# Kernel optimization log

Measured on AMD Instinct MI355X. Metric: run time of the kernel, lower is better.

## Reference

```python
import jax, jax.numpy as jnp
import numpy as np

D = 128          # embedding dim
N_INIT = 100000  # number of initial (axiom) clauses
L = 64           # topological levels of derived clauses
M = 4096         # derived clauses per level
N_THAX = 2000    # distinct axiom-name (thax) embeddings
N_SINE = 32      # sine-level embeddings
N_RULES = 256    # distinct inference rules (each with its own 2-ary MLP)
N_TOT = N_INIT + L * M


def setup_inputs() -> dict:
    key = jax.random.key(0)
    ks = jax.random.split(key, 10)
    rng = np.random.default_rng(0)
    # parents of level-l nodes point to any node created strictly earlier
    parents = np.stack(
        [rng.integers(0, N_INIT + l * M, size=(M, 2)) for l in range(L)]
    ).astype(np.int32)  # [L, M, 2]
    return {
        "thax_table": jax.random.normal(ks[0], (N_THAX, D), jnp.float32) * 0.1,
        "sine_table": jax.random.normal(ks[1], (N_SINE, D), jnp.float32) * 0.1,
        "rule_W": jax.random.normal(ks[2], (N_RULES, 2 * D, D), jnp.float32) * (1.0 / np.sqrt(2 * D)),
        "rule_b": jax.random.normal(ks[3], (N_RULES, D), jnp.float32) * 0.01,
        "eval_w": jax.random.normal(ks[4], (D,), jnp.float32) * (1.0 / np.sqrt(D)),
        "eval_b": jax.random.normal(ks[5], (1,), jnp.float32) * 0.01,
        "pos_vals": jax.random.uniform(ks[6], (N_TOT,), jnp.float32, 0.01, 1.0),
        "neg_vals": jax.random.uniform(ks[7], (N_TOT,), jnp.float32, 0.01, 1.0),
        "init_thax": jax.random.randint(ks[8], (N_INIT,), 0, N_THAX, jnp.int32),
        "init_sine": jax.random.randint(ks[9], (N_INIT,), 0, N_SINE, jnp.int32),
        "parents": jnp.asarray(parents),
        "rules": jnp.asarray(rng.integers(0, N_RULES, size=(L, M)).astype(np.int32)),
    }


def reference(thax_table, sine_table, rule_W, rule_b, eval_w, eval_b,
              pos_vals, neg_vals, init_thax, init_sine, parents, rules):
    n_init = init_thax.shape[0]
    n_lvl, m = rules.shape
    d = thax_table.shape[1]

    # init nodes: embed = init_embeds[thax]() + sine_embedder(sine)
    init_emb = thax_table[init_thax] + sine_table[init_sine]  # [N_INIT, D]
    store0 = jnp.concatenate(
        [init_emb, jnp.zeros((n_lvl * m, d), init_emb.dtype)], axis=0)  # [N_TOT, D]

    # deriv nodes, level by level: gather 2 parents, per-rule MLP (cat -> Linear -> ReLU)
    def step(store, xs):
        lvl, par, rul = xs                       # par: [M,2] int, rul: [M] int
        pe = store[par].reshape(m, 2 * d)        # gather parent embeddings
        emb = jax.nn.relu(jnp.einsum('mi,mio->mo', pe, rule_W[rul]) + rule_b[rul])
        store = jax.lax.dynamic_update_slice(store, emb, (n_init + lvl * m, 0))
        return store, None

    store, _ = jax.lax.scan(step, store0, (jnp.arange(n_lvl), parents, rules))

    # eval_net + weighted BCEWithLogits (pos_weight = tot_neg / tot_pos)
    logits = store @ eval_w + eval_b[0]          # [N_TOT]
    tot = pos_vals + neg_vals
    y = pos_vals / tot
    pw = jnp.sum(neg_vals) / jnp.sum(pos_vals)
    per_node = pw * y * jax.nn.softplus(-logits) + (1.0 - y) * jax.nn.softplus(logits)
    loss = jnp.sum(tot * per_node).reshape(1)
    posOK = jnp.sum(jnp.where(logits >= 0.0, pos_vals, 0.0))
    negOK = jnp.sum(jnp.where(logits < 0.0, neg_vals, 0.0))
    return (loss, posOK, negOK)
```

## Files before the change

kernel.cpp:

```cpp
#include <hip/hip_runtime.h>

#define D      128
#define NINIT  100000
#define LVLS   64
#define M      4096
#define NRULES 256
#define NTOT   (NINIT + LVLS * M)
#define NTHR   512
#define TILE   32

typedef __attribute__((ext_vector_type(8))) short short8;
typedef __attribute__((ext_vector_type(4))) float floatx4;

#define ST_OFF 256
#define SI_OFF (ST_OFF + (size_t)NTOT * D * 2)
#define RO_OFF (SI_OFF + (size_t)LVLS * M * 4)
#define FL_OFF (RO_OFF + (size_t)LVLS * (NRULES + 1) * 4)

#define CBAR() asm volatile("" ::: "memory")

__device__ __forceinline__ unsigned short f2bf(float x) {
  unsigned u = __float_as_uint(x);
  u += 0x7fffu + ((u >> 16) & 1u);
  return (unsigned short)(u >> 16);
}

__device__ __forceinline__ float softplusf(float x) {
  return fmaxf(x, 0.f) + log1pf(expf(-fabsf(x)));
}

__device__ __forceinline__ void st_sys(unsigned* p, unsigned v) {
  __hip_atomic_store(p, v, __ATOMIC_RELAXED, __HIP_MEMORY_SCOPE_SYSTEM);
}
__device__ __forceinline__ void st_sys64(unsigned long long* p,
                                         unsigned long long v) {
  __hip_atomic_store(p, v, __ATOMIC_RELAXED, __HIP_MEMORY_SCOPE_SYSTEM);
}
__device__ __forceinline__ unsigned ld_sys(const unsigned* p) {
  return __hip_atomic_load(p, __ATOMIC_RELAXED, __HIP_MEMORY_SCOPE_SYSTEM);
}

__device__ __forceinline__ void wait2(const unsigned* f0, bool n0,
                                      const unsigned* f1, bool n1) {
  if (__all(!(n0 || n1))) return;
  unsigned a0 = ld_sys(f0), a1 = ld_sys(f1);
  int guard = 1 << 16;
  for (;;) {
    unsigned b0 = ld_sys(f0), b1 = ld_sys(f1);
    bool ok = (!n0 || a0 != 0u) && (!n1 || a1 != 0u);
    if (__all(ok) || !--guard) break;
    a0 = ld_sys(f0); a1 = ld_sys(f1);
    ok = (!n0 || b0 != 0u) && (!n1 || b1 != 0u);
    if (__all(ok) || !--guard) break;
  }
  CBAR();
}

__device__ __forceinline__ void gbar_light(unsigned* bcnt, unsigned* bgen) {
  __syncthreads();
  if (threadIdx.x == 0) {
    unsigned g = ld_sys(bgen);
    unsigned v = __hip_atomic_fetch_add(bcnt, 1u, __ATOMIC_RELAXED,
                                        __HIP_MEMORY_SCOPE_SYSTEM);
    if (v == gridDim.x - 1) {
      st_sys(bcnt, 0u);
      st_sys(bgen, g + 1u);
    } else {
      int guard = 1 << 22;
      while (ld_sys(bgen) == g && --guard) __builtin_amdgcn_s_sleep(2);
    }
  }
  __syncthreads();
}

__device__ __forceinline__ bool adv_cursor(int r, const int* __restrict__ ro,
                                           int& l, int& t0, int& off, int& cnt) {
  t0 += TILE;
  while (t0 >= cnt) {
    if (++l >= LVLS) return false;
    off = ro[l * (NRULES + 1) + r];
    cnt = ro[l * (NRULES + 1) + r + 1] - off;
    t0 = 0;
  }
  return true;
}

__global__ __launch_bounds__(NTHR, 2) void fused_kernel(
    const float* __restrict__ thax_table, const float* __restrict__ sine_table,
    const float* __restrict__ rule_W, const float* __restrict__ rule_b,
    const float* __restrict__ eval_w, const float* __restrict__ eval_b,
    const float* __restrict__ pos, const float* __restrict__ neg,
    const int* __restrict__ init_thax, const int* __restrict__ init_sine,
    const int* __restrict__ parents,
    const int* __restrict__ rules,
    unsigned short* __restrict__ store, int* __restrict__ sorted_idx,
    int* __restrict__ rule_off, unsigned* __restrict__ flags,
    float* __restrict__ sums, unsigned* __restrict__ bvars,
    float* __restrict__ out) {
  __shared__ unsigned short pe[TILE * 264];
  __shared__ unsigned short ot[TILE * 136];
  __shared__ int s_sid[2][TILE];
  __shared__ int s_cnt[NRULES];
  __shared__ int s_base[NRULES + 1];
  __shared__ float racc[4];

  unsigned* bcnt = bvars;
  unsigned* bgen = bvars + 1;

  const int r = blockIdx.x;
  const int tid = threadIdx.x;
  const int wave = tid >> 6, lane = tid & 63;
  const int col = (wave << 4) + (lane & 15);
  const int node = tid >> 4;
  const int segq = tid & 15;

  float aP1 = 0.f, aP2 = 0.f, a_pos = 0.f, a_neg = 0.f;
  const float eb = eval_b[0];
  float w8[8];
  {
    float4 wA = ((const float4*)eval_w)[segq * 2];
    float4 wB = ((const float4*)eval_w)[segq * 2 + 1];
    w8[0] = wA.x; w8[1] = wA.y; w8[2] = wA.z; w8[3] = wA.w;
    w8[4] = wB.x; w8[5] = wB.y; w8[6] = wB.z; w8[7] = wB.w;
  }

  short8 bf[8];
  {
    const float* Wr = rule_W + (size_t)r * (2 * D * D);
    const int krow_base = (lane >> 4) * 8;
#pragma unroll
    for (int ks = 0; ks < 8; ++ks) {
      union { short8 s; unsigned short us[8]; } c;
#pragma unroll
      for (int j = 0; j < 8; ++j)
        c.us[j] = f2bf(Wr[(size_t)(ks * 32 + krow_base + j) * D + col]);
      bf[ks] = c.s;
    }
  }
  const float bias = rule_b[r * D + col];

  if (r < LVLS) {
    const int l = r;
    const int* rl = rules + (size_t)l * M;
    if (tid < NRULES) s_cnt[tid] = 0;
    __syncthreads();
    for (int m = tid; m < M; m += NTHR) atomicAdd(&s_cnt[rl[m]], 1);
    __syncthreads();
    int c = (tid < NRULES) ? s_cnt[tid] : 0;
    if (tid < NRULES) s_base[tid] = c;
    __syncthreads();
    for (int off = 1; off < NRULES; off <<= 1) {
      int t = (tid < NRULES && tid >= off) ? s_base[tid - off] : 0;
      __syncthreads();
      if (tid < NRULES) s_base[tid] += t;
      __syncthreads();
    }
    if (tid < NRULES) {
      int ex = s_base[tid] - c;
      st_sys((unsigned*)&rule_off[(size_t)l * (NRULES + 1) + tid],
             (unsigned)ex);
      s_cnt[tid] = ex;
    }
    if (tid == 0)
      st_sys((unsigned*)&rule_off[(size_t)l * (NRULES + 1) + NRULES],
             (unsigned)M);
    __syncthreads();
    for (int m = tid; m < M; m += NTHR) {
      int p = atomicAdd(&s_cnt[rl[m]], 1);
      st_sys((unsigned*)&sorted_idx[(size_t)l * M + p], (unsigned)m);
    }
  } else {
    const int gid3 = (r - LVLS) * NTHR + tid;
    const int gstride3 = (NRULES - LVLS) * NTHR;
    for (int idx = gid3; idx < NINIT * 16; idx += gstride3) {
      int nd = idx >> 4, sg = idx & 15;
      const float4* t = (const float4*)(thax_table + (size_t)init_thax[nd] * D) + sg * 2;
      const float4* s = (const float4*)(sine_table + (size_t)init_sine[nd] * D) + sg * 2;
      float4 a0 = t[0], a1 = t[1], b0 = s[0], b1 = s[1];
      float v[8] = {a0.x + b0.x, a0.y + b0.y, a0.z + b0.z, a0.w + b0.w,
                    a1.x + b1.x, a1.y + b1.y, a1.z + b1.z, a1.w + b1.w};
      unsigned p0 = (unsigned)f2bf(v[0]) | ((unsigned)f2bf(v[1]) << 16);
      unsigned p1 = (unsigned)f2bf(v[2]) | ((unsigned)f2bf(v[3]) << 16);
      unsigned p2 = (unsigned)f2bf(v[4]) | ((unsigned)f2bf(v[5]) << 16);
      unsigned p3 = (unsigned)f2bf(v[6]) | ((unsigned)f2bf(v[7]) << 16);
      unsigned long long* dst =
          (unsigned long long*)(store + (size_t)nd * D + sg * 8);
      st_sys64(dst + 0, (unsigned long long)p0 | ((unsigned long long)p1 << 32));
      st_sys64(dst + 1, (unsigned long long)p2 | ((unsigned long long)p3 << 32));

      float pd = v[0] * w8[0] + v[1] * w8[1] + v[2] * w8[2] + v[3] * w8[3] +
                 v[4] * w8[4] + v[5] * w8[5] + v[6] * w8[6] + v[7] * w8[7];
      pd += __shfl_xor(pd, 1, 64);
      pd += __shfl_xor(pd, 2, 64);
      pd += __shfl_xor(pd, 4, 64);
      pd += __shfl_xor(pd, 8, 64);
      if (sg == 0) {
        float logit = pd + eb;
        float pp = pos[nd], nn = neg[nd];
        float tot = pp + nn, y = pp / tot;
        aP1 += tot * y * softplusf(-logit);
        aP2 += tot * (1.f - y) * softplusf(logit);
        if (logit >= 0.f) a_pos += pp; else a_neg += nn;
      }
    }
    float sp = 0.f, sn = 0.f;
    for (int i = gid3; i < NTOT; i += gstride3) {
      sp += pos[i];
      sn += neg[i];
    }
    for (int m = 32; m; m >>= 1) {
      sp += __shfl_xor(sp, m, 64);
      sn += __shfl_xor(sn, m, 64);
    }
    if (lane == 0) {
      atomicAdd(&sums[0], sp);
      atomicAdd(&sums[1], sn);
    }
  }

  gbar_light(bcnt, bgen);

  const float pw = sums[1] / sums[0];

  int lL = -1, t0L = 0, offL = 0, cntL = 0;

  bool validA = adv_cursor(r, rule_off, lL, t0L, offL, cntL);
  int lA = lL, t0A = t0L, cntA = cntL;
  int parA0 = 0, parA1 = 0;
  bool lateA0 = false, lateA1 = false;
  unsigned reA0 = 1u, reA1 = 1u;
  float pPosA = 0.f, pNegA = 0.f;
  uint4 gA0 = {0, 0, 0, 0}, gA1 = {0, 0, 0, 0};
  if (validA) {
    int gj = t0A + node; if (gj > cntA - 1) gj = cntA - 1;
    int sid = sorted_idx[(size_t)lA * M + offL + gj];
    parA0 = parents[((size_t)lA * M + sid) * 2 + 0];
    parA1 = parents[((size_t)lA * M + sid) * 2 + 1];
    pPosA = pos[NINIT + lA * M + sid];
    pNegA = neg[NINIT + lA * M + sid];
    bool n0 = parA0 >= NINIT, n1 = parA1 >= NINIT;
    wait2(flags + (n0 ? parA0 - NINIT : 0), n0,
          flags + (n1 ? parA1 - NINIT : 0), n1);
    gA0 = *(const uint4*)(store + (size_t)parA0 * D + segq * 8);
    gA1 = *(const uint4*)(store + (size_t)parA1 * D + segq * 8);
    if (segq == 0) s_sid[0][node] = sid;
  }

  bool validB = validA && adv_cursor(r, rule_off, lL, t0L, offL, cntL);
  int lB = lL, t0B = t0L, cntB = cntL;
  int sidB = 0, parB0 = 0, parB1 = 0;
  unsigned fB0 = 1u, fB1 = 1u;
  float pPosB = 0.f, pNegB = 0.f;
  if (validB) {
    int gj = t0B + node; if (gj > cntB - 1) gj = cntB - 1;
    sidB = sorted_idx[(size_t)lB * M + offL + gj];
    parB0 = parents[((size_t)lB * M + sidB) * 2 + 0];
    parB1 = parents[((size_t)lB * M + sidB) * 2 + 1];
    fB0 = parB0 >= NINIT ? ld_sys(flags + (parB0 - NINIT)) : 1u;
    fB1 = parB1 >= NINIT ? ld_sys(flags + (parB1 - NINIT)) : 1u;
    pPosB = pos[NINIT + lB * M + sidB];
    pNegB = neg[NINIT + lB * M + sidB];
  }

  bool validC = validB && adv_cursor(r, rule_off, lL, t0L, offL, cntL);
  int lC = lL, t0C = t0L, cntC = cntL;
  int sidC = 0, parC0 = 0, parC1 = 0;
  if (validC) {
    int gj = t0C + node; if (gj > cntC - 1) gj = cntC - 1;
    sidC = sorted_idx[(size_t)lC * M + offL + gj];
    parC0 = parents[((size_t)lC * M + sidC) * 2 + 0];
    parC1 = parents[((size_t)lC * M + sidC) * 2 + 1];
  }

  bool validE = validC && adv_cursor(r, rule_off, lL, t0L, offL, cntL);
  int lE = lL, t0E = t0L, cntE = cntL;
  int sidE = 0;
  if (validE) {
    int gj = t0E + node; if (gj > cntE - 1) gj = cntE - 1;
    sidE = sorted_idx[(size_t)lE * M + offL + gj];
  }

  bool validF = validE && adv_cursor(r, rule_off, lL, t0L, offL, cntL);
  int lF = lL, t0F = t0L, offF = offL, cntF = cntL;

  int p = 0;
  while (validA) {
    {
      bool n0 = lateA0 && (reA0 == 0u);
      bool n1 = lateA1 && (reA1 == 0u);
      wait2(flags + (lateA0 ? parA0 - NINIT : 0), n0,
            flags + (lateA1 ? parA1 - NINIT : 0), n1);
      if (lateA0) gA0 = *(const uint4*)(store + (size_t)parA0 * D + segq * 8);
      if (lateA1) gA1 = *(const uint4*)(store + (size_t)parA1 * D + segq * 8);
    }

    *(uint4*)(pe + node * 264 + segq * 8) = gA0;
    *(uint4*)(pe + node * 264 + 128 + segq * 8) = gA1;
    __syncthreads();
    if (validB && segq == 0) s_sid[p ^ 1][node] = sidB;

    floatx4 acc0 = {0.f, 0.f, 0.f, 0.f}, acc1 = {0.f, 0.f, 0.f, 0.f};
#pragma unroll
    for (int ks = 0; ks < 8; ++ks) {
      short8 a0 = *(const short8*)(pe + (lane & 15) * 264 + ks * 32 + (lane >> 4) * 8);
      short8 a1 = *(const short8*)(pe + (16 + (lane & 15)) * 264 + ks * 32 + (lane >> 4) * 8);
      acc0 = __builtin_amdgcn_mfma_f32_16x16x32_bf16(a0, bf[ks], acc0, 0, 0, 0);
      acc1 = __builtin_amdgcn_mfma_f32_16x16x32_bf16(a1, bf[ks], acc1, 0, 0, 0);
    }
#pragma unroll
    for (int reg = 0; reg < 4; ++reg) {
      int row = (lane >> 4) * 4 + reg;
      float v0 = acc0[reg] + bias;
      float v1 = acc1[reg] + bias;
      ot[row * 136 + col] = f2bf(v0 > 0.f ? v0 : 0.f);
      ot[(16 + row) * 136 + col] = f2bf(v1 > 0.f ? v1 : 0.f);
    }
    __syncthreads();

    const int n_baseA = NINIT + lA * M;
#pragma unroll
    for (int k = 0; k < 4; ++k) {
      int nd = wave + 8 * k;
      if ((t0A + nd) < cntA)
        st_sys((unsigned*)(store + (size_t)(n_baseA + s_sid[p][nd]) * D) + lane,
               *(const unsigned*)(ot + nd * 136 + lane * 2));
    }
    CBAR();

    bool lateB0 = validB && parB0 >= NINIT && fB0 == 0u;
    bool lateB1 = validB && parB1 >= NINIT && fB1 == 0u;
    const unsigned short* ga0 =
        (validB && !lateB0) ? store + (size_t)parB0 * D : store;
    const unsigned short* ga1 =
        (validB && !lateB1) ? store + (size_t)parB1 * D : store;
    uint4 gB0 = *(const uint4*)(ga0 + segq * 8);
    uint4 gB1 = *(const uint4*)(ga1 + segq * 8);
    unsigned pol0 =
        ld_sys(flags + ((validC && parC0 >= NINIT) ? parC0 - NINIT : 0));
    unsigned pol1 =
        ld_sys(flags + ((validC && parC1 >= NINIT) ? parC1 - NINIT : 0));
    int idxC = NINIT + lC * M + sidC;
    float posC = pos[validC ? idxC : 0];
    float negC = neg[validC ? idxC : 0];
    int2 prE = *(const int2*)(parents +
                (validE ? (((size_t)lE * M + sidE) * 2) : 0));
    int cF = cntF > 0 ? cntF : 1;
    int gjF = t0F + node; if (gjF > cF - 1) gjF = cF - 1; if (gjF < 0) gjF = 0;
    int sidF = sorted_idx[validF ? ((size_t)lF * M + offF + gjF) : 0];
    unsigned reB0 = ld_sys(flags + (lateB0 ? parB0 - NINIT : 0));
    unsigned reB1 = ld_sys(flags + (lateB1 ? parB1 - NINIT : 0));
    CBAR();

    {
      const uint4 u = *(const uint4*)(ot + node * 136 + segq * 8);
      float pd = __uint_as_float(u.x << 16) * w8[0] +
                 __uint_as_float(u.x & 0xffff0000u) * w8[1] +
                 __uint_as_float(u.y << 16) * w8[2] +
                 __uint_as_float(u.y & 0xffff0000u) * w8[3] +
                 __uint_as_float(u.z << 16) * w8[4] +
                 __uint_as_float(u.z & 0xffff0000u) * w8[5] +
                 __uint_as_float(u.w << 16) * w8[6] +
                 __uint_as_float(u.w & 0xffff0000u) * w8[7];
      pd += __shfl_xor(pd, 1, 64);
      pd += __shfl_xor(pd, 2, 64);
      pd += __shfl_xor(pd, 4, 64);
      pd += __shfl_xor(pd, 8, 64);
      if (segq == 0 && (t0A + node) < cntA) {
        float logit = pd + eb;
        float tot = pPosA + pNegA, y = pPosA / tot;
        aP1 += tot * y * softplusf(-logit);
        aP2 += tot * (1.f - y) * softplusf(logit);
        if (logit >= 0.f) a_pos += pPosA; else a_neg += pNegA;
      }
    }

    asm volatile("s_waitcnt vmcnt(10)" ::: "memory");
    if (lane < 4) {
      int nd = wave + 8 * lane;
      int sidw = s_sid[p][nd];
      if ((t0A + nd) < cntA) st_sys(flags + lA * M + sidw, 1u);
    }
    CBAR();

    lateA0 = lateB0; lateA1 = lateB1;
    reA0 = reB0; reA1 = reB1;
    gA0 = gB0; gA1 = gB1;
    parA0 = parB0; parA1 = parB1;
    pPosA = pPosB; pNegA = pNegB;
    lA = lB; t0A = t0B; cntA = cntB; validA = validB;

    parB0 = parC0; parB1 = parC1; sidB = sidC;
    fB0 = (validC && parC0 >= NINIT) ? pol0 : 1u;
    fB1 = (validC && parC1 >= NINIT) ? pol1 : 1u;
    pPosB = posC; pNegB = negC;
    lB = lC; t0B = t0C; cntB = cntC; validB = validC;

    parC0 = validE ? prE.x : 0; parC1 = validE ? prE.y : 0;
    sidC = sidE;
    lC = lE; t0C = t0E; cntC = cntE; validC = validE;

    sidE = sidF;
    lE = lF; t0E = t0F; cntE = cntF; validE = validF;

    validF = validF && adv_cursor(r, rule_off, lL, t0L, offL, cntL);
    lF = lL; t0F = t0L; offF = offL; cntF = cntL;
    p ^= 1;
  }

  for (int m = 32; m; m >>= 1) {
    aP1   += __shfl_xor(aP1,   m, 64);
    aP2   += __shfl_xor(aP2,   m, 64);
    a_pos += __shfl_xor(a_pos, m, 64);
    a_neg += __shfl_xor(a_neg, m, 64);
  }
  if (tid == 0) { racc[0] = 0.f; racc[1] = 0.f; racc[2] = 0.f; racc[3] = 0.f; }
  __syncthreads();
  if (lane == 0) {
    atomicAdd(&racc[0], aP1);
    atomicAdd(&racc[1], aP2);
    atomicAdd(&racc[2], a_pos);
    atomicAdd(&racc[3], a_neg);
  }
  __syncthreads();
  if (tid == 0) {
    atomicAdd(&out[0], pw * racc[0] + racc[1]);
    atomicAdd(&out[1], racc[2]);
    atomicAdd(&out[2], racc[3]);
  }
}

extern "C" void kernel_launch(void* const* d_in, const int* in_sizes, int n_in,
                              void* d_out, int out_size, void* d_ws, size_t ws_size,
                              hipStream_t stream) {
  const float* thax_table = (const float*)d_in[0];
  const float* sine_table = (const float*)d_in[1];
  const float* rule_W     = (const float*)d_in[2];
  const float* rule_b     = (const float*)d_in[3];
  const float* eval_w     = (const float*)d_in[4];
  const float* eval_b     = (const float*)d_in[5];
  const float* pos_vals   = (const float*)d_in[6];
  const float* neg_vals   = (const float*)d_in[7];
  const int*   init_thax  = (const int*)d_in[8];
  const int*   init_sine  = (const int*)d_in[9];
  const int*   parents    = (const int*)d_in[10];
  const int*   rules      = (const int*)d_in[11];

  float* out = (float*)d_out;
  char* ws = (char*)d_ws;
  float* sums = (float*)ws;
  unsigned* bvars = (unsigned*)(ws + 128);
  unsigned short* store = (unsigned short*)(ws + ST_OFF);
  int* sorted_idx = (int*)(ws + SI_OFF);
  int* rule_off   = (int*)(ws + RO_OFF);
  unsigned* flags = (unsigned*)(ws + FL_OFF);

  (void)hipMemsetAsync(d_out, 0, 3 * sizeof(float), stream);
  (void)hipMemsetAsync(d_ws, 0, 256, stream);
  (void)hipMemsetAsync(ws + FL_OFF, 0, (size_t)LVLS * M * 4, stream);

  void* args[] = {&thax_table, &sine_table, &rule_W, &rule_b, &eval_w, &eval_b,
                  &pos_vals, &neg_vals, &init_thax, &init_sine, &parents,
                  &rules, &store, &sorted_idx, &rule_off, &flags, &sums,
                  &bvars, &out};
  (void)hipLaunchCooperativeKernel((void*)fused_kernel, dim3(NRULES),
                                   dim3(NTHR), args, 0, stream);
}
```

Measured before the change: 392.5 us.

## Rebalance init embedding work onto sort blocks and widen output stores

The per-level sort blocks now also take the tail of the initial-node embedding and eval work. Previously only the non-sort blocks handled it, and they had to finish before the grid barrier. The per-tile output store now has each lane write 16 bytes as two 64-bit system-scope stores covering all 32 rows at once, replacing four rounds of 32-bit stores. The flag polling loop is unrolled to a three-deep rotation of outstanding loads to hide load latency. Together these move the load balance before the barrier and change the store granularity of the hot loop.

```diff
diff --git a/kernel.cpp b/kernel.cpp
--- a/kernel.cpp
+++ b/kernel.cpp
@@ -8,6 +8,7 @@
 #define NTOT   (NINIT + LVLS * M)
 #define NTHR   512
 #define TILE   32
+#define SPLIT16 1280000
 
 typedef __attribute__((ext_vector_type(8))) short short8;
 typedef __attribute__((ext_vector_type(4))) float floatx4;
@@ -44,14 +45,16 @@
                                       const unsigned* f1, bool n1) {
   if (__all(!(n0 || n1))) return;
   unsigned a0 = ld_sys(f0), a1 = ld_sys(f1);
+  unsigned b0 = ld_sys(f0), b1 = ld_sys(f1);
   int guard = 1 << 16;
   for (;;) {
-    unsigned b0 = ld_sys(f0), b1 = ld_sys(f1);
-    bool ok = (!n0 || a0 != 0u) && (!n1 || a1 != 0u);
-    if (__all(ok) || !--guard) break;
+    unsigned c0 = ld_sys(f0), c1 = ld_sys(f1);
+    if (__all((!n0 || a0 != 0u) && (!n1 || a1 != 0u)) || !--guard) break;
     a0 = ld_sys(f0); a1 = ld_sys(f1);
-    ok = (!n0 || b0 != 0u) && (!n1 || b1 != 0u);
-    if (__all(ok) || !--guard) break;
+    if (__all((!n0 || b0 != 0u) && (!n1 || b1 != 0u)) || !--guard) break;
+    b0 = ld_sys(f0); b1 = ld_sys(f1);
+    if (__all((!n0 || c0 != 0u) && (!n1 || c1 != 0u)) || !--guard) break;
+    c0 = ld_sys(f0); c1 = ld_sys(f1);
   }
   CBAR();
 }
@@ -139,40 +142,8 @@
   }
   const float bias = rule_b[r * D + col];
 
-  if (r < LVLS) {
-    const int l = r;
-    const int* rl = rules + (size_t)l * M;
-    if (tid < NRULES) s_cnt[tid] = 0;
-    __syncthreads();
-    for (int m = tid; m < M; m += NTHR) atomicAdd(&s_cnt[rl[m]], 1);
-    __syncthreads();
-    int c = (tid < NRULES) ? s_cnt[tid] : 0;
-    if (tid < NRULES) s_base[tid] = c;
-    __syncthreads();
-    for (int off = 1; off < NRULES; off <<= 1) {
-      int t = (tid < NRULES && tid >= off) ? s_base[tid - off] : 0;
-      __syncthreads();
-      if (tid < NRULES) s_base[tid] += t;
-      __syncthreads();
-    }
-    if (tid < NRULES) {
-      int ex = s_base[tid] - c;
-      st_sys((unsigned*)&rule_off[(size_t)l * (NRULES + 1) + tid],
-             (unsigned)ex);
-      s_cnt[tid] = ex;
-    }
-    if (tid == 0)
-      st_sys((unsigned*)&rule_off[(size_t)l * (NRULES + 1) + NRULES],
-             (unsigned)M);
-    __syncthreads();
-    for (int m = tid; m < M; m += NTHR) {
-      int p = atomicAdd(&s_cnt[rl[m]], 1);
-      st_sys((unsigned*)&sorted_idx[(size_t)l * M + p], (unsigned)m);
-    }
-  } else {
-    const int gid3 = (r - LVLS) * NTHR + tid;
-    const int gstride3 = (NRULES - LVLS) * NTHR;
-    for (int idx = gid3; idx < NINIT * 16; idx += gstride3) {
+  auto init_body = [&](int idx0, int hi, int stride) {
+    for (int idx = idx0; idx < hi; idx += stride) {
       int nd = idx >> 4, sg = idx & 15;
       const float4* t = (const float4*)(thax_table + (size_t)init_thax[nd] * D) + sg * 2;
       const float4* s = (const float4*)(sine_table + (size_t)init_sine[nd] * D) + sg * 2;
@@ -203,6 +174,43 @@
         if (logit >= 0.f) a_pos += pp; else a_neg += nn;
       }
     }
+  };
+
+  if (r < LVLS) {
+    const int l = r;
+    const int* rl = rules + (size_t)l * M;
+    if (tid < NRULES) s_cnt[tid] = 0;
+    __syncthreads();
+    for (int m = tid; m < M; m += NTHR) atomicAdd(&s_cnt[rl[m]], 1);
+    __syncthreads();
+    int c = (tid < NRULES) ? s_cnt[tid] : 0;
+    if (tid < NRULES) s_base[tid] = c;
+    __syncthreads();
+    for (int off = 1; off < NRULES; off <<= 1) {
+      int t = (tid < NRULES && tid >= off) ? s_base[tid - off] : 0;
+      __syncthreads();
+      if (tid < NRULES) s_base[tid] += t;
+      __syncthreads();
+    }
+    if (tid < NRULES) {
+      int ex = s_base[tid] - c;
+      st_sys((unsigned*)&rule_off[(size_t)l * (NRULES + 1) + tid],
+             (unsigned)ex);
+      s_cnt[tid] = ex;
+    }
+    if (tid == 0)
+      st_sys((unsigned*)&rule_off[(size_t)l * (NRULES + 1) + NRULES],
+             (unsigned)M);
+    __syncthreads();
+    for (int m = tid; m < M; m += NTHR) {
+      int p = atomicAdd(&s_cnt[rl[m]], 1);
+      st_sys((unsigned*)&sorted_idx[(size_t)l * M + p], (unsigned)m);
+    }
+    init_body(SPLIT16 + r * NTHR + tid, NINIT * 16, LVLS * NTHR);
+  } else {
+    init_body((r - LVLS) * NTHR + tid, SPLIT16, (NRULES - LVLS) * NTHR);
+    const int gid3 = (r - LVLS) * NTHR + tid;
+    const int gstride3 = (NRULES - LVLS) * NTHR;
     float sp = 0.f, sn = 0.f;
     for (int i = gid3; i < NTOT; i += gstride3) {
       sp += pos[i];
@@ -318,12 +326,16 @@
     __syncthreads();
 
     const int n_baseA = NINIT + lA * M;
-#pragma unroll
-    for (int k = 0; k < 4; ++k) {
-      int nd = wave + 8 * k;
-      if ((t0A + nd) < cntA)
-        st_sys((unsigned*)(store + (size_t)(n_baseA + s_sid[p][nd]) * D) + lane,
-               *(const unsigned*)(ot + nd * 136 + lane * 2));
+    {
+      int nd = wave + 8 * (lane >> 4);
+      if ((t0A + nd) < cntA) {
+        uint4 v = *(const uint4*)(ot + nd * 136 + (lane & 15) * 8);
+        unsigned long long* dst =
+            (unsigned long long*)(store + (size_t)(n_baseA + s_sid[p][nd]) * D +
+                                  (lane & 15) * 8);
+        st_sys64(dst + 0, (unsigned long long)v.x | ((unsigned long long)v.y << 32));
+        st_sys64(dst + 1, (unsigned long long)v.z | ((unsigned long long)v.w << 32));
+      }
     }
     CBAR();
 
```

Result: no change. 392.9 us (+0.1%).
